# Optimization experiments

Hardware: AMD Instinct MI355X
Metric: run time of the kernel (lower is better)

The kernel has to match this reference:

```python
import jax, jax.numpy as jnp
import numpy as np

B, S, R, H, T = 256, 512, 128, 512, 96


def _lstm_cell(x, h, c, Wih, Whh, bih, bhh):
    # PyTorch LSTMCell: gates ordered i, f, g, o
    gates = x @ Wih.T + bih + h @ Whh.T + bhh
    i, f, g, o = jnp.split(gates, 4, axis=-1)
    i = jax.nn.sigmoid(i)
    f = jax.nn.sigmoid(f)
    g = jnp.tanh(g)
    o = jax.nn.sigmoid(o)
    c = f * c + i * g
    h = o * jnp.tanh(c)
    return h, c


def setup_inputs() -> dict:
    key = jax.random.key(0)
    ks = jax.random.split(key, 20)
    s = 0.05
    return {
        "enc_inputs": jax.random.normal(ks[0], (B, S), jnp.float32),
        "out_seq_len": T,
        "embed_W": jax.random.normal(ks[1], (R, 1), jnp.float32) * s,
        "embed_b": jax.random.normal(ks[2], (R,), jnp.float32) * s,
        "enc_Wih": jax.random.normal(ks[3], (4 * H, R), jnp.float32) * s,
        "enc_Whh": jax.random.normal(ks[4], (4 * H, H), jnp.float32) * s,
        "enc_bih": jax.random.normal(ks[5], (4 * H,), jnp.float32) * s,
        "enc_bhh": jax.random.normal(ks[6], (4 * H,), jnp.float32) * s,
        "dec_Wih": jax.random.normal(ks[7], (4 * H, 2 * H), jnp.float32) * s,
        "dec_Whh": jax.random.normal(ks[8], (4 * H, H), jnp.float32) * s,
        "dec_bih": jax.random.normal(ks[9], (4 * H,), jnp.float32) * s,
        "dec_bhh": jax.random.normal(ks[10], (4 * H,), jnp.float32) * s,
        "Wq": jax.random.normal(ks[11], (H, H), jnp.float32) * s,
        "bq": jax.random.normal(ks[12], (H,), jnp.float32) * s,
        "Wk": jax.random.normal(ks[13], (H, H), jnp.float32) * s,
        "bk": jax.random.normal(ks[14], (H,), jnp.float32) * s,
        "out_W": jax.random.normal(ks[15], (1, H), jnp.float32) * s,
        "out_b": jax.random.normal(ks[16], (1,), jnp.float32) * s,
    }


def reference(enc_inputs, out_seq_len, embed_W, embed_b,
              enc_Wih, enc_Whh, enc_bih, enc_bhh,
              dec_Wih, dec_Whh, dec_bih, dec_bhh,
              Wq, bq, Wk, bk, out_W, out_b):
    batch = enc_inputs.shape[0]
    hid = enc_Whh.shape[1]
    # embed: [B,S,1] -> [B,S,R]
    emb = enc_inputs[..., None] @ embed_W.T + embed_b
    xs = jnp.swapaxes(emb, 0, 1)  # [S,B,R]

    h0 = jnp.zeros((batch, hid), emb.dtype)
    c0 = jnp.zeros((batch, hid), emb.dtype)

    def enc_step(carry, x):
        h, c = carry
        h, c = _lstm_cell(x, h, c, enc_Wih, enc_Whh, enc_bih, enc_bhh)
        return (h, c), h

    (hN, cN), hs = jax.lax.scan(enc_step, (h0, c0), xs)
    in_hxs = jnp.swapaxes(hs, 0, 1)  # [B,S,H]

    # key projection is step-invariant; compute once (same math as per-step)
    kproj = in_hxs @ Wk.T + bk  # [B,S,H]

    def dec_step(carry, _):
        h, c = carry
        q = h @ Wq.T + bq                              # [B,H]
        scores = jnp.einsum('ba,bsa->bs', q, kproj)    # [B,S]
        w = jax.nn.softmax(scores, axis=-1)
        context = jnp.einsum('bs,bsh->bh', w, in_hxs)  # [B,H]
        x = jnp.concatenate([h, context], axis=-1)     # [B,2H]
        h, c = _lstm_cell(x, h, c, dec_Wih, dec_Whh, dec_bih, dec_bhh)
        return (h, c), h

    _, outs = jax.lax.scan(dec_step, (hN, cN), None, length=out_seq_len)
    outs = jnp.swapaxes(outs, 0, 1)  # [B,T,H]
    return jnp.squeeze(outs @ out_W.T + out_b, axis=-1)  # [B,T]
```

## Files before the change

kernel.cpp:

```cpp
#include <hip/hip_runtime.h>
#include <hip/hip_bf16.h>
#include <cstdint>
#include <cstddef>

#define BB   256
#define SS   512
#define RDIM 128
#define HH   512
#define TT   96

typedef unsigned int u32;
typedef _Float16 f16;
typedef __attribute__((ext_vector_type(8))) _Float16 f16x8;
typedef __attribute__((ext_vector_type(4))) float f32x4;

__device__ __forceinline__ float sigm(float x){ return 1.0f/(1.0f+__expf(-x)); }
__device__ __forceinline__ float tanh_f(float x){ return 1.0f - 2.0f/(__expf(2.0f*x)+1.0f); }
__device__ __forceinline__ float2 cvt2(u32 x){
  union { u32 u; f16 h[2]; } t; t.u = x;
  return make_float2((float)t.h[0], (float)t.h[1]);
}


__global__ void prep_uv(const float* __restrict__ Wih, const float* __restrict__ embW,
                        const float* __restrict__ embB, const float* __restrict__ bih,
                        const float* __restrict__ bhh, const float* __restrict__ dbih,
                        const float* __restrict__ dbhh,
                        float* __restrict__ u, float* __restrict__ v, float* __restrict__ bd){
  int n = blockIdx.x*256 + threadIdx.x;
  const float* row = Wih + (size_t)n*RDIM;
  float su = 0.f, sv = 0.f;
  for(int r=0;r<RDIM;r++){ float w = row[r]; su += w*embW[r]; sv += w*embB[r]; }
  u[n] = su;
  v[n] = sv + bih[n] + bhh[n];
  bd[n] = dbih[n] + dbhh[n];
}

__global__ void prep_wqk(const float* __restrict__ Wq, const float* __restrict__ Wk,
                         float* __restrict__ Wqk_t){
  __shared__ float wkc[HH];
  int n = blockIdx.x;
  for(int i=threadIdx.x;i<HH;i+=256) wkc[i] = Wk[(size_t)i*HH + n];
  __syncthreads();
  for(int a=threadIdx.x;a<HH;a+=256){
    float s = 0.f;
    for(int hp=0;hp<HH;hp++) s += Wq[(size_t)hp*HH + a]*wkc[hp];
    Wqk_t[(size_t)n*HH + a] = s;
  }
}

__global__ void prep_bqk(const float* __restrict__ bq, const float* __restrict__ Wk,
                         float* __restrict__ bqk){
  int n = blockIdx.x*256 + threadIdx.x;
  float s = 0.f;
  for(int hp=0;hp<HH;hp++) s += bq[hp]*Wk[(size_t)hp*HH + n];
  bqk[n] = s;
}

__global__ void prep_wenc(const float* __restrict__ Whh, const float* __restrict__ u,
                          const float* __restrict__ v, f16* __restrict__ Wfm){
  int nt = blockIdx.x, kk = blockIdx.y, L = threadIdx.x;
  int jb = nt>>2, ct = nt&3;
  int n = ct*HH + jb*16 + (L&15);
  int q = L>>4;
  union { f16 h[8]; uint4 u4; } z;
  if(kk < 16){
    const float* src = Whh + (size_t)n*HH + kk*32 + q*8;
    #pragma unroll
    for(int j=0;j<8;j++) z.h[j] = (f16)src[j];
  } else {
    #pragma unroll
    for(int j=0;j<8;j++) z.h[j] = (f16)0.0f;
    if(q==0){ z.h[0] = (f16)u[n]; z.h[1] = (f16)v[n]; }
  }
  *(uint4*)(Wfm + (((size_t)nt*17 + kk)*64 + L)*8) = z.u4;
}

__global__ void prep_wdec(const float* __restrict__ dWih, const float* __restrict__ dWhh,
                          const float* __restrict__ bd, f16* __restrict__ Wfm){
  int nt = blockIdx.x, kk = blockIdx.y, L = threadIdx.x;
  int jb = nt>>3, ct = nt&7;
  int n = (ct>>1)*HH + jb*32 + (ct&1)*16 + (L&15);
  int q = L>>4;
  union { f16 h[8]; uint4 u4; } z;
  if(kk < 32){
    int k0 = kk*32 + q*8;
    #pragma unroll
    for(int j=0;j<8;j++){
      float wv = dWih[(size_t)n*1024 + k0 + j];
      if(k0 + j < HH) wv += dWhh[(size_t)n*HH + k0 + j];
      z.h[j] = (f16)wv;
    }
  } else {
    #pragma unroll
    for(int j=0;j<8;j++) z.h[j] = (f16)0.0f;
    if(q==0) z.h[0] = (f16)bd[n];
  }
  *(uint4*)(Wfm + (((size_t)nt*33 + kk)*64 + L)*8) = z.u4;
}

__global__ void prep_wqfm(const float* __restrict__ Wqk_t, const float* __restrict__ bqk,
                          f16* __restrict__ Wfm){
  int nt = blockIdx.x, kk = blockIdx.y, L = threadIdx.x;
  int n = nt*16 + (L&15);
  int q = L>>4;
  union { f16 h[8]; uint4 u4; } z;
  if(kk < 16){
    const float* src = Wqk_t + (size_t)n*HH + kk*32 + q*8;
    #pragma unroll
    for(int j=0;j<8;j++) z.h[j] = (f16)src[j];
  } else {
    #pragma unroll
    for(int j=0;j<8;j++) z.h[j] = (f16)0.0f;
    if(q==0) z.h[0] = (f16)bqk[n];
  }
  *(uint4*)(Wfm + (((size_t)nt*17 + kk)*64 + L)*8) = z.u4;
}

#define STR 552

__launch_bounds__(256)
__global__ void enc_step(const f16* __restrict__ hin, f16* __restrict__ hout,
                         float* __restrict__ cbuf, const f16* __restrict__ Wfm,
                         const float* __restrict__ einp, f16* __restrict__ hx, int t){
  __shared__ f16 hsm[32*STR];
  __shared__ float gt[64][33];
  const int tid = threadIdx.x;
  const int b0 = blockIdx.x*32, jb = blockIdx.y;

  {
    int row = tid>>3, c0 = tid&7;
    const uint4* src = (const uint4*)(hin + (size_t)(b0+row)*HH);
    uint4* drow = (uint4*)(hsm + row*STR);
    #pragma unroll
    for(int i=0;i<8;i++) drow[c0 + 8*i] = src[c0 + 8*i];
  }
  if(tid < 128){
    int row = tid>>2, pc = tid&3;
    union { f16 h[8]; uint4 u4; } z;
    #pragma unroll
    for(int j=0;j<8;j++) z.h[j] = (f16)0.0f;
    if(pc==0){ z.h[0] = (f16)einp[(size_t)(b0+row)*SS + t]; z.h[1] = (f16)1.0f; }
    *((uint4*)(hsm + row*STR) + 64 + pc) = z.u4;
  }
  __syncthreads();

  const int lane = tid & 63, w = tid>>6;
  const int rt = w & 1, ctb = (w>>1)*2;
  const int m = lane & 15, q = lane>>4;
  f32x4 acc0 = {0.f,0.f,0.f,0.f}, acc1 = {0.f,0.f,0.f,0.f};
  const f16* arow = hsm + (rt*16 + m)*STR + q*8;
  const f16x8* bp0 = (const f16x8*)Wfm + ((size_t)(jb*4+ctb  )*17)*64 + lane;
  const f16x8* bp1 = (const f16x8*)Wfm + ((size_t)(jb*4+ctb+1)*17)*64 + lane;
  #pragma unroll
  for(int kk=0;kk<17;kk++){
    f16x8 a  = *(const f16x8*)(arow + kk*32);
    f16x8 b0 = bp0[kk*64];
    f16x8 b1 = bp1[kk*64];
    acc0 = __builtin_amdgcn_mfma_f32_16x16x32_f16(a, b0, acc0, 0,0,0);
    acc1 = __builtin_amdgcn_mfma_f32_16x16x32_f16(a, b1, acc1, 0,0,0);
  }
  #pragma unroll
  for(int r=0;r<4;r++){
    gt[(ctb  )*16 + m][rt*16 + q*4 + r] = acc0[r];
    gt[(ctb+1)*16 + m][rt*16 + q*4 + r] = acc1[r];
  }
  __syncthreads();

  #pragma unroll
  for(int qq=0;qq<2;qq++){
    int idx = tid + qq*256;
    int jc = idx & 15, rr = idx >> 4;
    float gi = gt[jc][rr];
    float gf = gt[16+jc][rr];
    float gg = gt[32+jc][rr];
    float go = gt[48+jc][rr];
    int b = b0 + rr, j = jb*16 + jc;
    size_t ci = (size_t)b*HH + j;
    float cv = sigm(gf)*cbuf[ci] + sigm(gi)*tanh_f(gg);
    cbuf[ci] = cv;
    float hv = sigm(go)*tanh_f(cv);
    hout[ci] = (f16)hv;
    hx[((size_t)b*SS + t)*HH + j] = (f16)hv;
  }
}

__launch_bounds__(256)
__global__ void qproj(const f16* __restrict__ hin, const f16* __restrict__ Wfm,
                      float* __restrict__ qt){
  __shared__ f16 hsm[32*STR];
  const int tid = threadIdx.x;
  const int b0 = blockIdx.x*32, jb = blockIdx.y;
  {
    int row = tid>>3, c0 = tid&7;
    const uint4* src = (const uint4*)(hin + (size_t)(b0+row)*HH);
    uint4* drow = (uint4*)(hsm + row*STR);
    #pragma unroll
    for(int i=0;i<8;i++) drow[c0 + 8*i] = src[c0 + 8*i];
  }
  if(tid < 128){
    int row = tid>>2, pc = tid&3;
    union { f16 h[8]; uint4 u4; } z;
    #pragma unroll
    for(int j=0;j<8;j++) z.h[j] = (f16)0.0f;
    if(pc==0) z.h[0] = (f16)1.0f;
    *((uint4*)(hsm + row*STR) + 64 + pc) = z.u4;
  }
  __syncthreads();

  const int lane = tid & 63, w = tid>>6;
  const int rt = w & 1, ctb = (w>>1)*2;
  const int m = lane & 15, q = lane>>4;
  f32x4 acc0 = {0.f,0.f,0.f,0.f}, acc1 = {0.f,0.f,0.f,0.f};
  const f16* arow = hsm + (rt*16 + m)*STR + q*8;
  const f16x8* bp0 = (const f16x8*)Wfm + ((size_t)(jb*4+ctb  )*17)*64 + lane;
  const f16x8* bp1 = (const f16x8*)Wfm + ((size_t)(jb*4+ctb+1)*17)*64 + lane;
  #pragma unroll
  for(int kk=0;kk<17;kk++){
    f16x8 a  = *(const f16x8*)(arow + kk*32);
    f16x8 b0 = bp0[kk*64];
    f16x8 b1 = bp1[kk*64];
    acc0 = __builtin_amdgcn_mfma_f32_16x16x32_f16(a, b0, acc0, 0,0,0);
    acc1 = __builtin_amdgcn_mfma_f32_16x16x32_f16(a, b1, acc1, 0,0,0);
  }
  #pragma unroll
  for(int r=0;r<4;r++){
    int b = b0 + rt*16 + q*4 + r;
    qt[(size_t)b*HH + jb*64 + (ctb  )*16 + m] = acc0[r];
    qt[(size_t)b*HH + jb*64 + (ctb+1)*16 + m] = acc1[r];
  }
}

__launch_bounds__(256)
__global__ void attn(const float* __restrict__ qt, const f16* __restrict__ hx,
                     f16* __restrict__ ctx){
  __shared__ unsigned short xs[32][520];
  __shared__ float sc[32];
  const int b = blockIdx.x, tid = threadIdx.x;
  const int seg = tid & 7;
  const int sp  = tid >> 3;

  float qreg[64];
  {
    const float4* qv = (const float4*)(qt + (size_t)b*HH + seg*64);
    #pragma unroll
    for(int i=0;i<16;i++){
      float4 v4 = qv[i];
      qreg[i*4+0]=v4.x; qreg[i*4+1]=v4.y; qreg[i*4+2]=v4.z; qreg[i*4+3]=v4.w;
    }
  }

  float m = -1e30f, l = 0.f, a0 = 0.f, a1 = 0.f;
  const uint4* src = (const uint4*)(hx + (size_t)b*SS*HH);

  for(int tile=0; tile<16; ++tile){
    __syncthreads();
    const uint4* tsrc = src + (size_t)tile*2048;
    #pragma unroll
    for(int kk=0;kk<8;kk++){
      uint4 vv = tsrc[kk*256 + tid];
      int e  = (kk*256 + tid)*8;
      int ss = e >> 9, hh = e & 511;
      *(uint4*)&xs[ss][hh] = vv;
    }
    __syncthreads();

    float p = 0.f;
    const uint4* xrow = (const uint4*)&xs[sp][seg*64];
    #pragma unroll
    for(int i=0;i<8;i++){
      uint4 vv = xrow[i];
      float2 t0 = cvt2(vv.x), t1 = cvt2(vv.y), t2 = cvt2(vv.z), t3 = cvt2(vv.w);
      p = fmaf(qreg[i*8+0], t0.x, p);
      p = fmaf(qreg[i*8+1], t0.y, p);
      p = fmaf(qreg[i*8+2], t1.x, p);
      p = fmaf(qreg[i*8+3], t1.y, p);
      p = fmaf(qreg[i*8+4], t2.x, p);
      p = fmaf(qreg[i*8+5], t2.y, p);
      p = fmaf(qreg[i*8+6], t3.x, p);
      p = fmaf(qreg[i*8+7], t3.y, p);
    }
    p += __shfl_xor(p, 1);
    p += __shfl_xor(p, 2);
    p += __shfl_xor(p, 4);
    if(seg == 0) sc[sp] = p;
    __syncthreads();

    float tmax = -1e30f;
    #pragma unroll
    for(int s2=0;s2<32;s2++) tmax = fmaxf(tmax, sc[s2]);
    float mnew  = fmaxf(m, tmax);
    float alpha = __expf(m - mnew);
    a0 *= alpha; a1 *= alpha; l *= alpha;
    #pragma unroll 4
    for(int s2=0;s2<32;s2++){
      float pv = __expf(sc[s2] - mnew);
      l += pv;
      u32 xv = *(const u32*)&xs[s2][2*tid];
      float2 xf = cvt2(xv);
      a0 = fmaf(pv, xf.x, a0);
      a1 = fmaf(pv, xf.y, a1);
    }
    m = mnew;
  }
  float inv = 1.0f/l;
  union { u32 u; f16 h[2]; } pk;
  pk.h[0] = (f16)(a0*inv); pk.h[1] = (f16)(a1*inv);
  *(u32*)(ctx + (size_t)b*HH + 2*tid) = pk.u;
}

#define STRD 1064

__launch_bounds__(256)
__global__ void dec_step(const f16* __restrict__ hin, f16* __restrict__ hout,
                         float* __restrict__ cbuf, const f16* __restrict__ ctxv,
                         const f16* __restrict__ Wfm, f16* __restrict__ hdec, int t){
  __shared__ f16 hsm[16*STRD];
  __shared__ float gt[128][17];
  const int tid = threadIdx.x;
  const int b0 = blockIdx.x*16, jb = blockIdx.y;

  {
    int row = tid>>4, c0 = tid&15;
    const uint4* srch = (const uint4*)(hin  + (size_t)(b0+row)*HH);
    const uint4* srcc = (const uint4*)(ctxv + (size_t)(b0+row)*HH);
    uint4* drow = (uint4*)(hsm + row*STRD);
    #pragma unroll
    for(int i=0;i<8;i++){
      int c = c0 + 16*i;
      drow[c] = (c < 64) ? srch[c] : srcc[c-64];
    }
  }
  if(tid < 64){
    int row = tid>>2, pc = tid&3;
    union { f16 h[8]; uint4 u4; } z;
    #pragma unroll
    for(int j=0;j<8;j++) z.h[j] = (f16)0.0f;
    if(pc==0) z.h[0] = (f16)1.0f;
    *((uint4*)(hsm + row*STRD) + 128 + pc) = z.u4;
  }
  __syncthreads();

  const int lane = tid & 63, w = tid>>6;
  const int ctb = w*2;
  const int m = lane & 15, q = lane>>4;
  f32x4 acc0 = {0.f,0.f,0.f,0.f}, acc1 = {0.f,0.f,0.f,0.f};
  const f16* arow = hsm + m*STRD + q*8;
  const f16x8* bp0 = (const f16x8*)Wfm + ((size_t)(jb*8+ctb  )*33)*64 + lane;
  const f16x8* bp1 = (const f16x8*)Wfm + ((size_t)(jb*8+ctb+1)*33)*64 + lane;
  #pragma unroll
  for(int kk=0;kk<33;kk++){
    f16x8 a  = *(const f16x8*)(arow + kk*32);
    f16x8 b0 = bp0[kk*64];
    f16x8 b1 = bp1[kk*64];
    acc0 = __builtin_amdgcn_mfma_f32_16x16x32_f16(a, b0, acc0, 0,0,0);
    acc1 = __builtin_amdgcn_mfma_f32_16x16x32_f16(a, b1, acc1, 0,0,0);
  }
  #pragma unroll
  for(int r=0;r<4;r++){
    gt[(ctb  )*16 + m][q*4 + r] = acc0[r];
    gt[(ctb+1)*16 + m][q*4 + r] = acc1[r];
  }
  __syncthreads();

  #pragma unroll
  for(int qq=0;qq<2;qq++){
    int idx = tid + qq*256;
    int jc = idx & 31, rr = idx >> 5;
    float gi = gt[jc][rr];
    float gf = gt[32+jc][rr];
    float gg = gt[64+jc][rr];
    float go = gt[96+jc][rr];
    int b = b0 + rr, j = jb*32 + jc;
    size_t ci = (size_t)b*HH + j;
    float cv = sigm(gf)*cbuf[ci] + sigm(gi)*tanh_f(gg);
    cbuf[ci] = cv;
    float hv = sigm(go)*tanh_f(cv);
    hout[ci] = (f16)hv;
    hdec[((size_t)t*BB + b)*HH + j] = (f16)hv;
  }
}

__launch_bounds__(256)
__global__ void final_out(const f16* __restrict__ hdec, const float* __restrict__ outW,
                          const float* __restrict__ outb, float* __restrict__ out){
  __shared__ float w[HH];
  int t = blockIdx.x;
  for(int i=threadIdx.x;i<HH;i+=256) w[i] = outW[i];
  __syncthreads();
  int b = threadIdx.x;
  const uint4* hp = (const uint4*)(hdec + ((size_t)t*BB + b)*HH);
  float s = 0.f;
  #pragma unroll 4
  for(int j=0;j<HH/8;j++){
    uint4 hv = hp[j];
    float2 t0 = cvt2(hv.x), t1 = cvt2(hv.y), t2 = cvt2(hv.z), t3 = cvt2(hv.w);
    s = fmaf(t0.x, w[j*8+0], s); s = fmaf(t0.y, w[j*8+1], s);
    s = fmaf(t1.x, w[j*8+2], s); s = fmaf(t1.y, w[j*8+3], s);
    s = fmaf(t2.x, w[j*8+4], s); s = fmaf(t2.y, w[j*8+5], s);
    s = fmaf(t3.x, w[j*8+6], s); s = fmaf(t3.y, w[j*8+7], s);
  }
  out[(size_t)b*TT + t] = s + outb[0];
}

extern "C" void kernel_launch(void* const* d_in, const int* in_sizes, int n_in,
                              void* d_out, int out_size, void* d_ws, size_t ws_size,
                              hipStream_t stream){
  const float* enc_in = (const float*)d_in[0];
  const float* embW = (const float*)d_in[2];
  const float* embB = (const float*)d_in[3];
  const float* eWih = (const float*)d_in[4];
  const float* eWhh = (const float*)d_in[5];
  const float* ebih = (const float*)d_in[6];
  const float* ebhh = (const float*)d_in[7];
  const float* dWih = (const float*)d_in[8];
  const float* dWhh = (const float*)d_in[9];
  const float* dbih = (const float*)d_in[10];
  const float* dbhh = (const float*)d_in[11];
  const float* Wq   = (const float*)d_in[12];
  const float* bq   = (const float*)d_in[13];
  const float* Wk   = (const float*)d_in[14];
  const float* outW = (const float*)d_in[16];
  const float* outb = (const float*)d_in[17];

  char* base = (char*)d_ws;
  f16* Wenc = (f16*)(base + 0);
  f16* Wdec = (f16*)(base + 2228224);
  f16* Wqf  = (f16*)(base + 6553600);
  f16* hb0  = (f16*)(base + 7110656);
  f16* hb1  = (f16*)(base + 7372800);
  f16* ctx  = (f16*)(base + 7634944);
  f16* hdec = (f16*)(base + 7897088);
  f16* hx   = (f16*)(base + 33062912);
  float* u     = (float*)(base + 167280640);
  float* v     = (float*)(base + 167288832);
  float* bd    = (float*)(base + 167297024);
  float* bqk   = (float*)(base + 167305216);
  float* Wqk_t = (float*)(base + 167307264);
  float* cb    = (float*)(base + 168355840);
  float* qt    = (float*)(base + 168880128);

  hipMemsetAsync(hb0, 0, (size_t)BB*HH*sizeof(f16), stream);
  hipMemsetAsync(cb,  0, (size_t)BB*HH*sizeof(float), stream);

  prep_uv  <<<8, 256, 0, stream>>>(eWih, embW, embB, ebih, ebhh, dbih, dbhh, u, v, bd);
  prep_bqk <<<2, 256, 0, stream>>>(bq, Wk, bqk);
  prep_wqk <<<512, 256, 0, stream>>>(Wq, Wk, Wqk_t);
  prep_wenc<<<dim3(128,17), 64, 0, stream>>>(eWhh, u, v, Wenc);
  prep_wdec<<<dim3(128,33), 64, 0, stream>>>(dWih, dWhh, bd, Wdec);
  prep_wqfm<<<dim3(32,17),  64, 0, stream>>>(Wqk_t, bqk, Wqf);

  f16* hbuf[2] = {hb0, hb1};
  for(int t=0;t<SS;t++){
    enc_step<<<dim3(8,32), 256, 0, stream>>>(hbuf[t&1], hbuf[(t+1)&1], cb,
                                             Wenc, enc_in, hx, t);
  }
  for(int t=0;t<TT;t++){
    qproj   <<<dim3(8,8),  256, 0, stream>>>(hbuf[t&1], Wqf, qt);
    attn    <<<256, 256, 0, stream>>>(qt, hx, ctx);
    dec_step<<<dim3(16,16),256, 0, stream>>>(hbuf[t&1], hbuf[(t+1)&1], cb, ctx,
                                             Wdec, hdec, t);
  }
  final_out<<<TT, 256, 0, stream>>>(hdec, outW, outb, (float*)d_out);
}
```

Baseline: 7.399 ms.

## Replace per-step kernel launches with persistent kernel using group barriers

Replaces the 512 encoder-step launches and 3×96 decoder launches with a single persistent kernel of 256 blocks. The blocks form 16 independent batch groups that synchronise through atomic counter barriers. Each block keeps its slice of the encoder and decoder weights in registers, keeps the cell state in registers, and fuses the output projection into the decoder step using shuffles and atomics. This removes launch overhead and repeated weight loads from global memory. In exchange it adds spin-wait barriers, heavy register pressure, and a requirement that all 256 blocks are resident at once.

```diff
diff --git a/kernel.cpp b/kernel.cpp
--- a/kernel.cpp
+++ b/kernel.cpp
@@ -8,6 +8,7 @@
 #define RDIM 128
 #define HH   512
 #define TT   96
+#define STRA 1040
 
 typedef unsigned int u32;
 typedef _Float16 f16;
@@ -60,347 +61,312 @@
 __global__ void prep_wenc(const float* __restrict__ Whh, const float* __restrict__ u,
                           const float* __restrict__ v, f16* __restrict__ Wfm){
   int nt = blockIdx.x, kk = blockIdx.y, L = threadIdx.x;
-  int jb = nt>>2, ct = nt&3;
-  int n = ct*HH + jb*16 + (L&15);
-  int q = L>>4;
+  int jb = nt>>3, ct = nt&7;
+  int n = (ct>>1)*HH + jb*32 + (ct&1)*16 + (L&15);
+  int qq = L>>4;
   union { f16 h[8]; uint4 u4; } z;
   if(kk < 16){
-    const float* src = Whh + (size_t)n*HH + kk*32 + q*8;
+    const float* src = Whh + (size_t)n*HH + kk*32 + qq*8;
     #pragma unroll
     for(int j=0;j<8;j++) z.h[j] = (f16)src[j];
   } else {
     #pragma unroll
     for(int j=0;j<8;j++) z.h[j] = (f16)0.0f;
-    if(q==0){ z.h[0] = (f16)u[n]; z.h[1] = (f16)v[n]; }
-  }
-  *(uint4*)(Wfm + (((size_t)nt*17 + kk)*64 + L)*8) = z.u4;
+    if(qq==0){ z.h[0] = (f16)u[n]; z.h[1] = (f16)v[n]; }
+  }
+  ((uint4*)Wfm)[((size_t)nt*17 + kk)*64 + L] = z.u4;
 }
 
 __global__ void prep_wdec(const float* __restrict__ dWih, const float* __restrict__ dWhh,
-                          const float* __restrict__ bd, f16* __restrict__ Wfm){
+                          f16* __restrict__ Wfm){
   int nt = blockIdx.x, kk = blockIdx.y, L = threadIdx.x;
   int jb = nt>>3, ct = nt&7;
   int n = (ct>>1)*HH + jb*32 + (ct&1)*16 + (L&15);
-  int q = L>>4;
+  int qq = L>>4;
+  int k0 = kk*32 + qq*8;
   union { f16 h[8]; uint4 u4; } z;
-  if(kk < 32){
-    int k0 = kk*32 + q*8;
-    #pragma unroll
-    for(int j=0;j<8;j++){
-      float wv = dWih[(size_t)n*1024 + k0 + j];
-      if(k0 + j < HH) wv += dWhh[(size_t)n*HH + k0 + j];
-      z.h[j] = (f16)wv;
-    }
-  } else {
-    #pragma unroll
-    for(int j=0;j<8;j++) z.h[j] = (f16)0.0f;
-    if(q==0) z.h[0] = (f16)bd[n];
-  }
-  *(uint4*)(Wfm + (((size_t)nt*33 + kk)*64 + L)*8) = z.u4;
-}
-
-__global__ void prep_wqfm(const float* __restrict__ Wqk_t, const float* __restrict__ bqk,
-                          f16* __restrict__ Wfm){
+  #pragma unroll
+  for(int j=0;j<8;j++){
+    float wv = dWih[(size_t)n*1024 + k0 + j];
+    if(k0 + j < HH) wv += dWhh[(size_t)n*HH + k0 + j];
+    z.h[j] = (f16)wv;
+  }
+  ((uint4*)Wfm)[((size_t)nt*32 + kk)*64 + L] = z.u4;
+}
+
+__global__ void prep_wqfm(const float* __restrict__ Wqk_t, f16* __restrict__ Wfm){
   int nt = blockIdx.x, kk = blockIdx.y, L = threadIdx.x;
   int n = nt*16 + (L&15);
-  int q = L>>4;
+  int qq = L>>4;
   union { f16 h[8]; uint4 u4; } z;
-  if(kk < 16){
-    const float* src = Wqk_t + (size_t)n*HH + kk*32 + q*8;
-    #pragma unroll
-    for(int j=0;j<8;j++) z.h[j] = (f16)src[j];
-  } else {
-    #pragma unroll
-    for(int j=0;j<8;j++) z.h[j] = (f16)0.0f;
-    if(q==0) z.h[0] = (f16)bqk[n];
-  }
-  *(uint4*)(Wfm + (((size_t)nt*17 + kk)*64 + L)*8) = z.u4;
-}
-
-#define STR 552
-
-__launch_bounds__(256)
-__global__ void enc_step(const f16* __restrict__ hin, f16* __restrict__ hout,
-                         float* __restrict__ cbuf, const f16* __restrict__ Wfm,
-                         const float* __restrict__ einp, f16* __restrict__ hx, int t){
-  __shared__ f16 hsm[32*STR];
-  __shared__ float gt[64][33];
+  const float* src = Wqk_t + (size_t)n*HH + kk*32 + qq*8;
+  #pragma unroll
+  for(int j=0;j<8;j++) z.h[j] = (f16)src[j];
+  ((uint4*)Wfm)[((size_t)nt*16 + kk)*64 + L] = z.u4;
+}
+
+__device__ __forceinline__ void groupbar(u32* slot){
+  __syncthreads();
+  if(threadIdx.x == 0){
+    __hip_atomic_fetch_add(slot, 1u, __ATOMIC_RELEASE, __HIP_MEMORY_SCOPE_AGENT);
+    while(__hip_atomic_load(slot, __ATOMIC_ACQUIRE, __HIP_MEMORY_SCOPE_AGENT) < 16u)
+      __builtin_amdgcn_s_sleep(1);
+  }
+  __syncthreads();
+}
+
+__global__ void __launch_bounds__(256, 1)
+persist(const float* __restrict__ einp, const f16* __restrict__ Wenc,
+        const f16* __restrict__ Wdec, const f16* __restrict__ Wqf,
+        const float* __restrict__ bd, const float* __restrict__ bqk,
+        f16* __restrict__ hb0, f16* __restrict__ hb1, f16* __restrict__ hx,
+        f16* __restrict__ ctxg, float* __restrict__ qt,
+        const float* __restrict__ outW, const float* __restrict__ outb,
+        float* __restrict__ out, u32* __restrict__ bar){
+  __shared__ f16 smA[16*STRA];
+  __shared__ float gt[128][17];
+  __shared__ float sc[32];
+
   const int tid = threadIdx.x;
-  const int b0 = blockIdx.x*32, jb = blockIdx.y;
-
+  const int gid = blockIdx.x >> 4;
+  const int role = blockIdx.x & 15;
+  const int b0 = gid*16;
+  const int lane = tid & 63, w = tid >> 6;
+  const int m = lane & 15, q = lane >> 4;
+  const int jL = tid & 31, rr = tid >> 5;
+  u32* gbar = bar + (size_t)gid*1024;
+  f16* hb[2] = {hb0, hb1};
+
+  f16x8 Be0[17], Be1[17];
   {
-    int row = tid>>3, c0 = tid&7;
-    const uint4* src = (const uint4*)(hin + (size_t)(b0+row)*HH);
-    uint4* drow = (uint4*)(hsm + row*STR);
-    #pragma unroll
-    for(int i=0;i<8;i++) drow[c0 + 8*i] = src[c0 + 8*i];
-  }
-  if(tid < 128){
-    int row = tid>>2, pc = tid&3;
-    union { f16 h[8]; uint4 u4; } z;
-    #pragma unroll
-    for(int j=0;j<8;j++) z.h[j] = (f16)0.0f;
-    if(pc==0){ z.h[0] = (f16)einp[(size_t)(b0+row)*SS + t]; z.h[1] = (f16)1.0f; }
-    *((uint4*)(hsm + row*STR) + 64 + pc) = z.u4;
-  }
-  __syncthreads();
-
-  const int lane = tid & 63, w = tid>>6;
-  const int rt = w & 1, ctb = (w>>1)*2;
-  const int m = lane & 15, q = lane>>4;
-  f32x4 acc0 = {0.f,0.f,0.f,0.f}, acc1 = {0.f,0.f,0.f,0.f};
-  const f16* arow = hsm + (rt*16 + m)*STR + q*8;
-  const f16x8* bp0 = (const f16x8*)Wfm + ((size_t)(jb*4+ctb  )*17)*64 + lane;
-  const f16x8* bp1 = (const f16x8*)Wfm + ((size_t)(jb*4+ctb+1)*17)*64 + lane;
-  #pragma unroll
-  for(int kk=0;kk<17;kk++){
-    f16x8 a  = *(const f16x8*)(arow + kk*32);
-    f16x8 b0 = bp0[kk*64];
-    f16x8 b1 = bp1[kk*64];
-    acc0 = __builtin_amdgcn_mfma_f32_16x16x32_f16(a, b0, acc0, 0,0,0);
-    acc1 = __builtin_amdgcn_mfma_f32_16x16x32_f16(a, b1, acc1, 0,0,0);
-  }
-  #pragma unroll
-  for(int r=0;r<4;r++){
-    gt[(ctb  )*16 + m][rt*16 + q*4 + r] = acc0[r];
-    gt[(ctb+1)*16 + m][rt*16 + q*4 + r] = acc1[r];
-  }
-  __syncthreads();
-
-  #pragma unroll
-  for(int qq=0;qq<2;qq++){
-    int idx = tid + qq*256;
-    int jc = idx & 15, rr = idx >> 4;
-    float gi = gt[jc][rr];
-    float gf = gt[16+jc][rr];
-    float gg = gt[32+jc][rr];
-    float go = gt[48+jc][rr];
-    int b = b0 + rr, j = jb*16 + jc;
-    size_t ci = (size_t)b*HH + j;
-    float cv = sigm(gf)*cbuf[ci] + sigm(gi)*tanh_f(gg);
-    cbuf[ci] = cv;
-    float hv = sigm(go)*tanh_f(cv);
-    hout[ci] = (f16)hv;
-    hx[((size_t)b*SS + t)*HH + j] = (f16)hv;
-  }
-}
-
-__launch_bounds__(256)
-__global__ void qproj(const f16* __restrict__ hin, const f16* __restrict__ Wfm,
-                      float* __restrict__ qt){
-  __shared__ f16 hsm[32*STR];
-  const int tid = threadIdx.x;
-  const int b0 = blockIdx.x*32, jb = blockIdx.y;
+    int nt0 = role*8 + 2*w;
+    #pragma unroll
+    for(int kk=0;kk<17;kk++){
+      Be0[kk] = ((const f16x8*)Wenc)[((size_t)nt0*17 + kk)*64 + lane];
+      Be1[kk] = ((const f16x8*)Wenc)[((size_t)(nt0+1)*17 + kk)*64 + lane];
+    }
+  }
+  float c0 = 0.f, c1 = 0.f;
+
+  for(int t=0; t<SS; ++t){
+    {
+      int row = tid>>4, cc = tid&15;
+      const uint4* src = (const uint4*)(hb[t&1] + (size_t)(b0+row)*HH);
+      uint4* drow = (uint4*)(smA + row*STRA);
+      #pragma unroll
+      for(int i=0;i<4;i++) drow[cc + 16*i] = src[cc + 16*i];
+    }
+    if(tid < 64){
+      int row = tid>>2, pc = tid&3;
+      union { f16 h[8]; uint4 u4; } z;
+      #pragma unroll
+      for(int j=0;j<8;j++) z.h[j] = (f16)0.0f;
+      if(pc==0){ z.h[0] = (f16)einp[(size_t)(b0+row)*SS + t]; z.h[1] = (f16)1.0f; }
+      ((uint4*)(smA + row*STRA))[64 + pc] = z.u4;
+    }
+    __syncthreads();
+
+    f32x4 a0 = {0.f,0.f,0.f,0.f}, a1 = {0.f,0.f,0.f,0.f};
+    const f16* arow = smA + m*STRA + q*8;
+    #pragma unroll
+    for(int kk=0;kk<17;kk++){
+      f16x8 a = *(const f16x8*)(arow + kk*32);
+      a0 = __builtin_amdgcn_mfma_f32_16x16x32_f16(a, Be0[kk], a0, 0,0,0);
+      a1 = __builtin_amdgcn_mfma_f32_16x16x32_f16(a, Be1[kk], a1, 0,0,0);
+    }
+    #pragma unroll
+    for(int r=0;r<4;r++){
+      gt[w*32 + m][q*4+r]      = a0[r];
+      gt[w*32 + 16 + m][q*4+r] = a1[r];
+    }
+    __syncthreads();
+
+    #pragma unroll
+    for(int qq=0;qq<2;qq++){
+      int bl = rr + qq*8;
+      float gi = gt[jL][bl];
+      float gf = gt[32+jL][bl];
+      float gg = gt[64+jL][bl];
+      float go = gt[96+jL][bl];
+      float& cr = qq ? c1 : c0;
+      float cv = sigm(gf)*cr + sigm(gi)*tanh_f(gg);
+      cr = cv;
+      float hv = sigm(go)*tanh_f(cv);
+      int b = b0 + bl, j = role*32 + jL;
+      hb[(t+1)&1][(size_t)b*HH + j] = (f16)hv;
+      hx[((size_t)b*SS + t)*HH + j] = (f16)hv;
+    }
+    groupbar(&gbar[t]);
+  }
+
+  f16x8 Bd0[32], Bd1[32];
   {
-    int row = tid>>3, c0 = tid&7;
-    const uint4* src = (const uint4*)(hin + (size_t)(b0+row)*HH);
-    uint4* drow = (uint4*)(hsm + row*STR);
-    #pragma unroll
-    for(int i=0;i<8;i++) drow[c0 + 8*i] = src[c0 + 8*i];
-  }
-  if(tid < 128){
-    int row = tid>>2, pc = tid&3;
-    union { f16 h[8]; uint4 u4; } z;
-    #pragma unroll
-    for(int j=0;j<8;j++) z.h[j] = (f16)0.0f;
-    if(pc==0) z.h[0] = (f16)1.0f;
-    *((uint4*)(hsm + row*STR) + 64 + pc) = z.u4;
-  }
-  __syncthreads();
-
-  const int lane = tid & 63, w = tid>>6;
-  const int rt = w & 1, ctb = (w>>1)*2;
-  const int m = lane & 15, q = lane>>4;
-  f32x4 acc0 = {0.f,0.f,0.f,0.f}, acc1 = {0.f,0.f,0.f,0.f};
-  const f16* arow = hsm + (rt*16 + m)*STR + q*8;
-  const f16x8* bp0 = (const f16x8*)Wfm + ((size_t)(jb*4+ctb  )*17)*64 + lane;
-  const f16x8* bp1 = (const f16x8*)Wfm + ((size_t)(jb*4+ctb+1)*17)*64 + lane;
-  #pragma unroll
-  for(int kk=0;kk<17;kk++){
-    f16x8 a  = *(const f16x8*)(arow + kk*32);
-    f16x8 b0 = bp0[kk*64];
-    f16x8 b1 = bp1[kk*64];
-    acc0 = __builtin_amdgcn_mfma_f32_16x16x32_f16(a, b0, acc0, 0,0,0);
-    acc1 = __builtin_amdgcn_mfma_f32_16x16x32_f16(a, b1, acc1, 0,0,0);
-  }
-  #pragma unroll
-  for(int r=0;r<4;r++){
-    int b = b0 + rt*16 + q*4 + r;
-    qt[(size_t)b*HH + jb*64 + (ctb  )*16 + m] = acc0[r];
-    qt[(size_t)b*HH + jb*64 + (ctb+1)*16 + m] = acc1[r];
-  }
-}
-
-__launch_bounds__(256)
-__global__ void attn(const float* __restrict__ qt, const f16* __restrict__ hx,
-                     f16* __restrict__ ctx){
-  __shared__ unsigned short xs[32][520];
-  __shared__ float sc[32];
-  const int b = blockIdx.x, tid = threadIdx.x;
-  const int seg = tid & 7;
-  const int sp  = tid >> 3;
-
-  float qreg[64];
-  {
-    const float4* qv = (const float4*)(qt + (size_t)b*HH + seg*64);
-    #pragma unroll
-    for(int i=0;i<16;i++){
-      float4 v4 = qv[i];
-      qreg[i*4+0]=v4.x; qreg[i*4+1]=v4.y; qreg[i*4+2]=v4.z; qreg[i*4+3]=v4.w;
-    }
-  }
-
-  float m = -1e30f, l = 0.f, a0 = 0.f, a1 = 0.f;
-  const uint4* src = (const uint4*)(hx + (size_t)b*SS*HH);
-
-  for(int tile=0; tile<16; ++tile){
+    int nt0 = role*8 + 2*w;
+    #pragma unroll
+    for(int kk=0;kk<32;kk++){
+      Bd0[kk] = ((const f16x8*)Wdec)[((size_t)nt0*32 + kk)*64 + lane];
+      Bd1[kk] = ((const f16x8*)Wdec)[((size_t)(nt0+1)*32 + kk)*64 + lane];
+    }
+  }
+  const float bd0v = bd[w*HH + role*32 + m];
+  const float bd1v = bd[w*HH + role*32 + 16 + m];
+  const float bqv  = (w < 2) ? bqk[role*32 + w*16 + m] : 0.f;
+  const float oW0 = outW[role*32 + jL];
+  const float ob0 = outb[0];
+  const int battn = b0 + role;
+
+  for(int t=0; t<TT; ++t){
+    {
+      int row = tid>>4, cc = tid&15;
+      const uint4* src = (const uint4*)(hb[t&1] + (size_t)(b0+row)*HH);
+      uint4* drow = (uint4*)(smA + row*STRA);
+      #pragma unroll
+      for(int i=0;i<4;i++) drow[cc + 16*i] = src[cc + 16*i];
+    }
     __syncthreads();
-    const uint4* tsrc = src + (size_t)tile*2048;
-    #pragma unroll
-    for(int kk=0;kk<8;kk++){
-      uint4 vv = tsrc[kk*256 + tid];
-      int e  = (kk*256 + tid)*8;
-      int ss = e >> 9, hh = e & 511;
-      *(uint4*)&xs[ss][hh] = vv;
+    if(w < 2){
+      f32x4 aq = {0.f,0.f,0.f,0.f};
+      int nt = role*2 + w;
+      const f16* arow = smA + m*STRA + q*8;
+      #pragma unroll
+      for(int kk=0;kk<16;kk++){
+        f16x8 a = *(const f16x8*)(arow + kk*32);
+        f16x8 bf = ((const f16x8*)Wqf)[((size_t)nt*16 + kk)*64 + lane];
+        aq = __builtin_amdgcn_mfma_f32_16x16x32_f16(a, bf, aq, 0,0,0);
+      }
+      #pragma unroll
+      for(int r=0;r<4;r++)
+        qt[(size_t)(b0 + q*4 + r)*HH + role*32 + w*16 + m] = aq[r] + bqv;
+    }
+    groupbar(&gbar[SS + t*3]);
+
+    {
+      unsigned short* xs = (unsigned short*)smA;
+      const int seg = tid & 7, sp = tid >> 3;
+      float qreg[64];
+      {
+        const float4* qv = (const float4*)(qt + (size_t)battn*HH + seg*64);
+        #pragma unroll
+        for(int i=0;i<16;i++){
+          float4 v4 = qv[i];
+          qreg[i*4+0]=v4.x; qreg[i*4+1]=v4.y; qreg[i*4+2]=v4.z; qreg[i*4+3]=v4.w;
+        }
+      }
+      float mm = -1e30f, ll = 0.f, aa0 = 0.f, aa1 = 0.f;
+      const uint4* src = (const uint4*)(hx + (size_t)battn*SS*HH);
+      for(int tile=0; tile<16; ++tile){
+        __syncthreads();
+        const uint4* tsrc = src + (size_t)tile*2048;
+        #pragma unroll
+        for(int kk=0;kk<8;kk++){
+          uint4 vv = tsrc[kk*256 + tid];
+          int e  = (kk*256 + tid)*8;
+          int ss = e >> 9, hh = e & 511;
+          *(uint4*)&xs[ss*520 + hh] = vv;
+        }
+        __syncthreads();
+        float p = 0.f;
+        const uint4* xrow = (const uint4*)&xs[sp*520 + seg*64];
+        #pragma unroll
+        for(int i=0;i<8;i++){
+          uint4 vv = xrow[i];
+          float2 t0 = cvt2(vv.x), t1 = cvt2(vv.y), t2 = cvt2(vv.z), t3 = cvt2(vv.w);
+          p = fmaf(qreg[i*8+0], t0.x, p);
+          p = fmaf(qreg[i*8+1], t0.y, p);
+          p = fmaf(qreg[i*8+2], t1.x, p);
+          p = fmaf(qreg[i*8+3], t1.y, p);
+          p = fmaf(qreg[i*8+4], t2.x, p);
+          p = fmaf(qreg[i*8+5], t2.y, p);
+          p = fmaf(qreg[i*8+6], t3.x, p);
+          p = fmaf(qreg[i*8+7], t3.y, p);
+        }
+        p += __shfl_xor(p, 1);
+        p += __shfl_xor(p, 2);
+        p += __shfl_xor(p, 4);
+        if(seg == 0) sc[sp] = p;
+        __syncthreads();
+        float tmax = -1e30f;
+        #pragma unroll
+        for(int s2=0;s2<32;s2++) tmax = fmaxf(tmax, sc[s2]);
+        float mnew  = fmaxf(mm, tmax);
+        float alpha = __expf(mm - mnew);
+        aa0 *= alpha; aa1 *= alpha; ll *= alpha;
+        #pragma unroll 4
+        for(int s2=0;s2<32;s2++){
+          float pv = __expf(sc[s2] - mnew);
+          ll += pv;
+          u32 xv = *(const u32*)&xs[s2*520 + 2*tid];
+          float2 xf = cvt2(xv);
+          aa0 = fmaf(pv, xf.x, aa0);
+          aa1 = fmaf(pv, xf.y, aa1);
+        }
+        mm = mnew;
+      }
+      float inv = 1.0f/ll;
+      union { u32 u; f16 h[2]; } pk;
+      pk.h[0] = (f16)(aa0*inv); pk.h[1] = (f16)(aa1*inv);
+      *(u32*)(ctxg + (size_t)battn*HH + 2*tid) = pk.u;
+    }
+    groupbar(&gbar[SS + t*3 + 1]);
+
+    {
+      int row = tid>>4, cc = tid&15;
+      const uint4* srch = (const uint4*)(hb[t&1]  + (size_t)(b0+row)*HH);
+      const uint4* srcc = (const uint4*)(ctxg     + (size_t)(b0+row)*HH);
+      uint4* drow = (uint4*)(smA + row*STRA);
+      #pragma unroll
+      for(int i=0;i<8;i++){
+        int c = cc + 16*i;
+        drow[c] = (c < 64) ? srch[c] : srcc[c-64];
+      }
     }
     __syncthreads();
 
-    float p = 0.f;
-    const uint4* xrow = (const uint4*)&xs[sp][seg*64];
-    #pragma unroll
-    for(int i=0;i<8;i++){
-      uint4 vv = xrow[i];
-      float2 t0 = cvt2(vv.x), t1 = cvt2(vv.y), t2 = cvt2(vv.z), t3 = cvt2(vv.w);
-      p = fmaf(qreg[i*8+0], t0.x, p);
-      p = fmaf(qreg[i*8+1], t0.y, p);
-      p = fmaf(qreg[i*8+2], t1.x, p);
-      p = fmaf(qreg[i*8+3], t1.y, p);
-      p = fmaf(qreg[i*8+4], t2.x, p);
-      p = fmaf(qreg[i*8+5], t2.y, p);
-      p = fmaf(qreg[i*8+6], t3.x, p);
-      p = fmaf(qreg[i*8+7], t3.y, p);
-    }
-    p += __shfl_xor(p, 1);
-    p += __shfl_xor(p, 2);
-    p += __shfl_xor(p, 4);
-    if(seg == 0) sc[sp] = p;
+    f32x4 a0 = {bd0v,bd0v,bd0v,bd0v}, a1 = {bd1v,bd1v,bd1v,bd1v};
+    {
+      const f16* arow = smA + m*STRA + q*8;
+      #pragma unroll
+      for(int kk=0;kk<32;kk++){
+        f16x8 a = *(const f16x8*)(arow + kk*32);
+        a0 = __builtin_amdgcn_mfma_f32_16x16x32_f16(a, Bd0[kk], a0, 0,0,0);
+        a1 = __builtin_amdgcn_mfma_f32_16x16x32_f16(a, Bd1[kk], a1, 0,0,0);
+      }
+    }
+    #pragma unroll
+    for(int r=0;r<4;r++){
+      gt[w*32 + m][q*4+r]      = a0[r];
+      gt[w*32 + 16 + m][q*4+r] = a1[r];
+    }
     __syncthreads();
 
-    float tmax = -1e30f;
-    #pragma unroll
-    for(int s2=0;s2<32;s2++) tmax = fmaxf(tmax, sc[s2]);
-    float mnew  = fmaxf(m, tmax);
-    float alpha = __expf(m - mnew);
-    a0 *= alpha; a1 *= alpha; l *= alpha;
-    #pragma unroll 4
-    for(int s2=0;s2<32;s2++){
-      float pv = __expf(sc[s2] - mnew);
-      l += pv;
-      u32 xv = *(const u32*)&xs[s2][2*tid];
-      float2 xf = cvt2(xv);
-      a0 = fmaf(pv, xf.x, a0);
-      a1 = fmaf(pv, xf.y, a1);
-    }
-    m = mnew;
-  }
-  float inv = 1.0f/l;
-  union { u32 u; f16 h[2]; } pk;
-  pk.h[0] = (f16)(a0*inv); pk.h[1] = (f16)(a1*inv);
-  *(u32*)(ctx + (size_t)b*HH + 2*tid) = pk.u;
-}
-
-#define STRD 1064
-
-__launch_bounds__(256)
-__global__ void dec_step(const f16* __restrict__ hin, f16* __restrict__ hout,
-                         float* __restrict__ cbuf, const f16* __restrict__ ctxv,
-                         const f16* __restrict__ Wfm, f16* __restrict__ hdec, int t){
-  __shared__ f16 hsm[16*STRD];
-  __shared__ float gt[128][17];
-  const int tid = threadIdx.x;
-  const int b0 = blockIdx.x*16, jb = blockIdx.y;
-
-  {
-    int row = tid>>4, c0 = tid&15;
-    const uint4* srch = (const uint4*)(hin  + (size_t)(b0+row)*HH);
-    const uint4* srcc = (const uint4*)(ctxv + (size_t)(b0+row)*HH);
-    uint4* drow = (uint4*)(hsm + row*STRD);
-    #pragma unroll
-    for(int i=0;i<8;i++){
-      int c = c0 + 16*i;
-      drow[c] = (c < 64) ? srch[c] : srcc[c-64];
-    }
-  }
-  if(tid < 64){
-    int row = tid>>2, pc = tid&3;
-    union { f16 h[8]; uint4 u4; } z;
-    #pragma unroll
-    for(int j=0;j<8;j++) z.h[j] = (f16)0.0f;
-    if(pc==0) z.h[0] = (f16)1.0f;
-    *((uint4*)(hsm + row*STRD) + 128 + pc) = z.u4;
-  }
-  __syncthreads();
-
-  const int lane = tid & 63, w = tid>>6;
-  const int ctb = w*2;
-  const int m = lane & 15, q = lane>>4;
-  f32x4 acc0 = {0.f,0.f,0.f,0.f}, acc1 = {0.f,0.f,0.f,0.f};
-  const f16* arow = hsm + m*STRD + q*8;
-  const f16x8* bp0 = (const f16x8*)Wfm + ((size_t)(jb*8+ctb  )*33)*64 + lane;
-  const f16x8* bp1 = (const f16x8*)Wfm + ((size_t)(jb*8+ctb+1)*33)*64 + lane;
-  #pragma unroll
-  for(int kk=0;kk<33;kk++){
-    f16x8 a  = *(const f16x8*)(arow + kk*32);
-    f16x8 b0 = bp0[kk*64];
-    f16x8 b1 = bp1[kk*64];
-    acc0 = __builtin_amdgcn_mfma_f32_16x16x32_f16(a, b0, acc0, 0,0,0);
-    acc1 = __builtin_amdgcn_mfma_f32_16x16x32_f16(a, b1, acc1, 0,0,0);
-  }
-  #pragma unroll
-  for(int r=0;r<4;r++){
-    gt[(ctb  )*16 + m][q*4 + r] = acc0[r];
-    gt[(ctb+1)*16 + m][q*4 + r] = acc1[r];
-  }
-  __syncthreads();
-
-  #pragma unroll
-  for(int qq=0;qq<2;qq++){
-    int idx = tid + qq*256;
-    int jc = idx & 31, rr = idx >> 5;
-    float gi = gt[jc][rr];
-    float gf = gt[32+jc][rr];
-    float gg = gt[64+jc][rr];
-    float go = gt[96+jc][rr];
-    int b = b0 + rr, j = jb*32 + jc;
-    size_t ci = (size_t)b*HH + j;
-    float cv = sigm(gf)*cbuf[ci] + sigm(gi)*tanh_f(gg);
-    cbuf[ci] = cv;
-    float hv = sigm(go)*tanh_f(cv);
-    hout[ci] = (f16)hv;
-    hdec[((size_t)t*BB + b)*HH + j] = (f16)hv;
-  }
-}
-
-__launch_bounds__(256)
-__global__ void final_out(const f16* __restrict__ hdec, const float* __restrict__ outW,
-                          const float* __restrict__ outb, float* __restrict__ out){
-  __shared__ float w[HH];
-  int t = blockIdx.x;
-  for(int i=threadIdx.x;i<HH;i+=256) w[i] = outW[i];
-  __syncthreads();
-  int b = threadIdx.x;
-  const uint4* hp = (const uint4*)(hdec + ((size_t)t*BB + b)*HH);
-  float s = 0.f;
-  #pragma unroll 4
-  for(int j=0;j<HH/8;j++){
-    uint4 hv = hp[j];
-    float2 t0 = cvt2(hv.x), t1 = cvt2(hv.y), t2 = cvt2(hv.z), t3 = cvt2(hv.w);
-    s = fmaf(t0.x, w[j*8+0], s); s = fmaf(t0.y, w[j*8+1], s);
-    s = fmaf(t1.x, w[j*8+2], s); s = fmaf(t1.y, w[j*8+3], s);
-    s = fmaf(t2.x, w[j*8+4], s); s = fmaf(t2.y, w[j*8+5], s);
-    s = fmaf(t3.x, w[j*8+6], s); s = fmaf(t3.y, w[j*8+7], s);
-  }
-  out[(size_t)b*TT + t] = s + outb[0];
+    float po[2];
+    #pragma unroll
+    for(int qq=0;qq<2;qq++){
+      int bl = rr + qq*8;
+      float gi = gt[jL][bl];
+      float gf = gt[32+jL][bl];
+      float gg = gt[64+jL][bl];
+      float go = gt[96+jL][bl];
+      float& cr = qq ? c1 : c0;
+      float cv = sigm(gf)*cr + sigm(gi)*tanh_f(gg);
+      cr = cv;
+      float hv = sigm(go)*tanh_f(cv);
+      int b = b0 + bl, j = role*32 + jL;
+      hb[(t+1)&1][(size_t)b*HH + j] = (f16)hv;
+      po[qq] = hv * oW0;
+    }
+    #pragma unroll
+    for(int k=1;k<32;k<<=1){
+      po[0] += __shfl_xor(po[0], k);
+      po[1] += __shfl_xor(po[1], k);
+    }
+    if(jL == 0){
+      float bias = (role == 0) ? ob0 : 0.f;
+      atomicAdd(&out[(size_t)(b0 + rr)*TT + t],     po[0] + bias);
+      atomicAdd(&out[(size_t)(b0 + rr + 8)*TT + t], po[1] + bias);
+    }
+    groupbar(&gbar[SS + t*3 + 2]);
+  }
 }
 
 extern "C" void kernel_launch(void* const* d_in, const int* in_sizes, int n_in,
@@ -424,42 +390,33 @@
   const float* outb = (const float*)d_in[17];
 
   char* base = (char*)d_ws;
-  f16* Wenc = (f16*)(base + 0);
-  f16* Wdec = (f16*)(base + 2228224);
-  f16* Wqf  = (f16*)(base + 6553600);
-  f16* hb0  = (f16*)(base + 7110656);
-  f16* hb1  = (f16*)(base + 7372800);
-  f16* ctx  = (f16*)(base + 7634944);
-  f16* hdec = (f16*)(base + 7897088);
-  f16* hx   = (f16*)(base + 33062912);
-  float* u     = (float*)(base + 167280640);
-  float* v     = (float*)(base + 167288832);
-  float* bd    = (float*)(base + 167297024);
-  float* bqk   = (float*)(base + 167305216);
-  float* Wqk_t = (float*)(base + 167307264);
-  float* cb    = (float*)(base + 168355840);
-  float* qt    = (float*)(base + 168880128);
+  f16* Wenc   = (f16*)(base + 0);
+  f16* Wdec   = (f16*)(base + 2228224);
+  f16* Wqf    = (f16*)(base + 6422528);
+  f16* hb0    = (f16*)(base + 6946816);
+  f16* hb1    = (f16*)(base + 7208960);
+  f16* ctxg   = (f16*)(base + 7471104);
+  float* qt   = (float*)(base + 7733248);
+  float* Wqk_t= (float*)(base + 8257536);
+  float* u    = (float*)(base + 9306112);
+  float* v    = (float*)(base + 9314304);
+  float* bd   = (float*)(base + 9322496);
+  float* bqk  = (float*)(base + 9330688);
+  u32* bar    = (u32*)(base + 9332736);
+  f16* hx     = (f16*)(base + 9437184);
 
   hipMemsetAsync(hb0, 0, (size_t)BB*HH*sizeof(f16), stream);
-  hipMemsetAsync(cb,  0, (size_t)BB*HH*sizeof(float), stream);
+  hipMemsetAsync(bar, 0, 16*1024*sizeof(u32), stream);
+  hipMemsetAsync(d_out, 0, (size_t)out_size*sizeof(float), stream);
 
   prep_uv  <<<8, 256, 0, stream>>>(eWih, embW, embB, ebih, ebhh, dbih, dbhh, u, v, bd);
   prep_bqk <<<2, 256, 0, stream>>>(bq, Wk, bqk);
   prep_wqk <<<512, 256, 0, stream>>>(Wq, Wk, Wqk_t);
   prep_wenc<<<dim3(128,17), 64, 0, stream>>>(eWhh, u, v, Wenc);
-  prep_wdec<<<dim3(128,33), 64, 0, stream>>>(dWih, dWhh, bd, Wdec);
-  prep_wqfm<<<dim3(32,17),  64, 0, stream>>>(Wqk_t, bqk, Wqf);
-
-  f16* hbuf[2] = {hb0, hb1};
-  for(int t=0;t<SS;t++){
-    enc_step<<<dim3(8,32), 256, 0, stream>>>(hbuf[t&1], hbuf[(t+1)&1], cb,
-                                             Wenc, enc_in, hx, t);
-  }
-  for(int t=0;t<TT;t++){
-    qproj   <<<dim3(8,8),  256, 0, stream>>>(hbuf[t&1], Wqf, qt);
-    attn    <<<256, 256, 0, stream>>>(qt, hx, ctx);
-    dec_step<<<dim3(16,16),256, 0, stream>>>(hbuf[t&1], hbuf[(t+1)&1], cb, ctx,
-                                             Wdec, hdec, t);
-  }
-  final_out<<<TT, 256, 0, stream>>>(hdec, outW, outb, (float*)d_out);
-}
+  prep_wdec<<<dim3(128,32), 64, 0, stream>>>(dWih, dWhh, Wdec);
+  prep_wqfm<<<dim3(32,16),  64, 0, stream>>>(Wqk_t, Wqf);
+
+  persist<<<256, 256, 0, stream>>>(enc_in, Wenc, Wdec, Wqf, bd, bqk,
+                                   hb0, hb1, hx, ctxg, qt,
+                                   outW, outb, (float*)d_out, bar);
+}
```

Result: slower. 15.43 ms (+108.5%).
